# Kernel tuning notes

Hardware: AMD Instinct MI355X
Metric: run time of the kernel (lower is better)

## Reference

```python
import jax, jax.numpy as jnp
import numpy as np

N_SR = 50000; N_TG = 50000; DIM = 256; VAL_DIM = 300; ATT_NUM = 1001
N_VAL = 100000; E_ATTR = 200000; E_EDGE = 400000; N_SEED = 10000


def _build_adj(rng, n, e):
    # replicate preprocess_adj: symmetrize, add self-loops, coalesce + clamp(values,1)
    edges = rng.integers(0, n, size=(e, 2))
    und = np.concatenate([edges, edges[:, ::-1]], axis=0)
    loops = np.repeat(np.arange(n)[:, None], 2, axis=1)
    uniq = np.unique(np.concatenate([und, loops], axis=0), axis=0)  # coalesced binary adj
    return jnp.asarray(uniq[:, 0], jnp.int32), jnp.asarray(uniq[:, 1], jnp.int32)


def _xavier(k, shape):
    fan_in, fan_out = shape[0], shape[-1]
    s = jnp.sqrt(6.0 / (fan_in + fan_out)).astype(jnp.float32)
    return jax.random.uniform(k, shape, jnp.float32, -1.0, 1.0) * s


def setup_inputs():
    rng = np.random.default_rng(0)
    ks = jax.random.split(jax.random.key(0), 10)

    def triples(n_ent):
        return jnp.asarray(np.stack([rng.integers(0, n_ent, E_ATTR),
                                     rng.integers(0, N_VAL, E_ATTR),
                                     rng.integers(0, ATT_NUM, E_ATTR)], axis=1), jnp.int32)

    r_sr, c_sr = _build_adj(rng, N_SR, E_EDGE)
    r_tg, c_tg = _build_adj(rng, N_TG, E_EDGE)
    return {
        'ent_seed_sr': jnp.asarray(rng.integers(0, N_SR, N_SEED), jnp.int32),
        'ent_seed_tg': jnp.asarray(rng.integers(0, N_TG, N_SEED), jnp.int32),
        'attribute_triples_sr': triples(N_SR),
        'attribute_triples_tg': triples(N_TG),
        'adj_rows_sr': r_sr, 'adj_cols_sr': c_sr,
        'adj_rows_tg': r_tg, 'adj_cols_tg': c_tg,
        'att_feats': _xavier(ks[0], (ATT_NUM, DIM)),
        'val_feats': jax.random.normal(ks[1], (N_VAL, VAL_DIM), jnp.float32),
        'ent_feats_sr': _xavier(ks[2], (N_SR, DIM)),
        'ent_feats_tg': _xavier(ks[3], (N_TG, DIM)),
        'a_w': _xavier(ks[4], (2 * DIM, 1)).reshape(-1),
        'a_b': jnp.zeros((1,), jnp.float32),
        'W_enc': _xavier(ks[5], (DIM + VAL_DIM, DIM)),
        'gcn_w1': _xavier(ks[6], (DIM, DIM)),
        'gcn_b1': jnp.zeros((DIM,), jnp.float32),
        'gcn_w2': _xavier(ks[7], (DIM, DIM)),
        'gcn_b2': jnp.zeros((DIM,), jnp.float32),
    }


def attributed_encoder(triples, att_feats, val_feats, ent_feats, a_w, a_b, W_enc):
    h, val, att = triples[:, 0], triples[:, 1], triples[:, 2]
    n = ent_feats.shape[0]
    # edge attention score: Linear(cat(ent[h], att[att])) -> exp(leaky_relu(.))
    score = jnp.concatenate([ent_feats[h], att_feats[att]], axis=-1) @ a_w + a_b[0]  # [E]
    score = jnp.exp(jax.nn.leaky_relu(score, negative_slope=0.2))
    row_sum = jax.ops.segment_sum(score, h, num_segments=n)      # sparse softmax denom
    p = score / row_sum[h]                                       # [E]
    av = jnp.concatenate([att_feats[att], val_feats[val]], axis=-1) @ W_enc  # [E, DIM]
    agg = jax.ops.segment_sum(av * p[:, None], h, num_segments=n)
    return jax.nn.elu(agg + ent_feats)


def gcn_layer(rows, cols, feats, w, b, act):
    n = feats.shape[0]
    agg = jax.ops.segment_sum(feats[cols], rows, num_segments=n)           # A @ feats
    deg = jax.ops.segment_sum(jnp.ones(rows.shape, feats.dtype), rows, num_segments=n)
    h = act((agg / deg[:, None]) @ w + b)
    return feats + h  # residual, dims match


def _l2norm(x):
    return x / jnp.maximum(jnp.linalg.norm(x, axis=-1, keepdims=True), 1e-12)


def reference(ent_seed_sr, ent_seed_tg, attribute_triples_sr, attribute_triples_tg,
              adj_rows_sr, adj_cols_sr, adj_rows_tg, adj_cols_tg,
              att_feats, val_feats, ent_feats_sr, ent_feats_tg,
              a_w, a_b, W_enc, gcn_w1, gcn_b1, gcn_w2, gcn_b2):
    fs = attributed_encoder(attribute_triples_sr, att_feats, val_feats, ent_feats_sr, a_w, a_b, W_enc)
    ft = attributed_encoder(attribute_triples_tg, att_feats, val_feats, ent_feats_tg, a_w, a_b, W_enc)
    fs = gcn_layer(adj_rows_sr, adj_cols_sr, fs, gcn_w1, gcn_b1, jax.nn.relu)
    ft = gcn_layer(adj_rows_tg, adj_cols_tg, ft, gcn_w1, gcn_b1, jax.nn.relu)
    fs = gcn_layer(adj_rows_sr, adj_cols_sr, fs, gcn_w2, gcn_b2, lambda x: x)
    ft = gcn_layer(adj_rows_tg, adj_cols_tg, ft, gcn_w2, gcn_b2, lambda x: x)
    fs = _l2norm(fs)
    ft = _l2norm(ft)
    return fs[ent_seed_sr], ft[ent_seed_tg], fs, ft
```

## Files before the change

kernel.cpp:

```cpp
#include <hip/hip_runtime.h>
#include <math.h>

#define DIM 256
#define VAL_DIM 300

typedef __attribute__((ext_vector_type(8))) short short8;
typedef __attribute__((ext_vector_type(4))) float fx4;
typedef _Float16 f16;
typedef __attribute__((ext_vector_type(4))) _Float16 h4;

__device__ __forceinline__ short f2bf(float x) {
    unsigned u = __float_as_uint(x);
    unsigned r = (u + 0x7fff + ((u >> 16) & 1)) >> 16;
    return (short)r;
}
__device__ __forceinline__ float bf2f(short h) {
    return __uint_as_float(((unsigned)(unsigned short)h) << 16);
}

__global__ void k_split_b(const float* __restrict__ W, short* __restrict__ Bhi,
                          short* __restrict__ Blo, int Kreal, int Kp, int Ncols) {
    int idx = blockIdx.x * 256 + threadIdx.x;
    int total = (Ncols / 16) * (Kp / 32) * 64;
    if (idx >= total) return;
    int lane = idx & 63;
    int kt = (idx >> 6) % (Kp / 32);
    int nt = (idx >> 6) / (Kp / 32);
    int n = nt * 16 + (lane & 15);
    int kbase = kt * 32 + ((lane >> 4) & 3) * 8;
    short h[8], l[8];
#pragma unroll
    for (int j = 0; j < 8; ++j) {
        int k = kbase + j;
        float x = (k < Kreal) ? W[(size_t)k * Ncols + n] : 0.f;
        short hh = f2bf(x);
        float r = x - bf2f(hh);
        h[j] = hh;
        l[j] = f2bf(r);
    }
    size_t base = (size_t)idx * 8;
#pragma unroll
    for (int j = 0; j < 8; ++j) { Bhi[base + j] = h[j]; Blo[base + j] = l[j]; }
}

template <int MODE>
__global__ void k_gemm(const float* __restrict__ A, const short* __restrict__ Bhi,
                       const short* __restrict__ Blo, const float* __restrict__ bias,
                       float* __restrict__ Out, f16* __restrict__ Out16, int M, int K, int Kp) {
    __shared__ short Ah[8 * 512];
    __shared__ short Al[8 * 512];
    const int m0 = blockIdx.x * 64;
    const int tid = threadIdx.x;
    const int wave = tid >> 6;
    const int lane = tid & 63;
    const int wm = wave >> 2;
    const int wn = wave & 3;
    fx4 acc[2][4] = {};

    for (int pk = 0; pk < Kp; pk += 64) {
        {
            int ss = tid;
            int mt = ss >> 7;
            int ks = (ss >> 6) & 1;
            int ln = ss & 63;
            int row = m0 + mt * 16 + (ln & 15);
            int kk = pk + ks * 32 + ((ln >> 4) & 3) * 8;
            float v[8];
            if (row < M && kk + 8 <= K) {
                fx4 u0 = *(const fx4*)&A[(size_t)row * K + kk];
                fx4 u1 = *(const fx4*)&A[(size_t)row * K + kk + 4];
                v[0] = u0[0]; v[1] = u0[1]; v[2] = u0[2]; v[3] = u0[3];
                v[4] = u1[0]; v[5] = u1[1]; v[6] = u1[2]; v[7] = u1[3];
            } else {
#pragma unroll
                for (int j = 0; j < 8; ++j)
                    v[j] = (row < M && kk + j < K) ? A[(size_t)row * K + kk + j] : 0.f;
            }
            short8 h8, l8;
#pragma unroll
            for (int j = 0; j < 8; ++j) {
                short hh = f2bf(v[j]);
                h8[j] = hh;
                l8[j] = f2bf(v[j] - bf2f(hh));
            }
            *(short8*)&Ah[(mt * 2 + ks) * 512 + ln * 8] = h8;
            *(short8*)&Al[(mt * 2 + ks) * 512 + ln * 8] = l8;
        }
        __syncthreads();
#pragma unroll
        for (int ks = 0; ks < 2; ++ks) {
            int kglob = pk + ks * 32;
            short8 ah[2], al[2], bh[4], bl[4];
#pragma unroll
            for (int t = 0; t < 2; ++t) {
                ah[t] = *(short8*)&Ah[((wm * 2 + t) * 2 + ks) * 512 + lane * 8];
                al[t] = *(short8*)&Al[((wm * 2 + t) * 2 + ks) * 512 + lane * 8];
            }
#pragma unroll
            for (int t = 0; t < 4; ++t) {
                int ntg = wn * 4 + t;
                size_t fb = ((size_t)(ntg * (Kp >> 5) + (kglob >> 5))) * 512 + lane * 8;
                bh[t] = *(const short8*)&Bhi[fb];
                bl[t] = *(const short8*)&Blo[fb];
            }
#pragma unroll
            for (int i = 0; i < 2; ++i)
#pragma unroll
                for (int j = 0; j < 4; ++j) {
                    acc[i][j] = __builtin_amdgcn_mfma_f32_16x16x32_bf16(ah[i], bh[j], acc[i][j], 0, 0, 0);
                    acc[i][j] = __builtin_amdgcn_mfma_f32_16x16x32_bf16(ah[i], bl[j], acc[i][j], 0, 0, 0);
                    acc[i][j] = __builtin_amdgcn_mfma_f32_16x16x32_bf16(al[i], bh[j], acc[i][j], 0, 0, 0);
                }
        }
        __syncthreads();
    }
    const int quad = lane >> 4;
    const int cl = lane & 15;
#pragma unroll
    for (int i = 0; i < 2; ++i) {
        int rbase = m0 + (wm * 2 + i) * 16 + quad * 4;
#pragma unroll
        for (int j = 0; j < 4; ++j) {
            int col = (wn * 4 + j) * 16 + cl;
            float bb = (MODE == 0) ? 0.f : bias[col];
#pragma unroll
            for (int r = 0; r < 4; ++r) {
                int row = rbase + r;
                if (row >= M) continue;
                size_t idx = (size_t)row * DIM + col;
                if (MODE == 0) {
                    Out16[idx] = (f16)acc[i][j][r];
                } else if (MODE == 1) {
                    float h = fmaxf(acc[i][j][r] + bb, 0.f);
                    float v = Out[idx] + h;
                    Out[idx] = v;
                    Out16[idx] = (f16)v;
                } else {
                    Out[idx] += acc[i][j][r] + bb;
                }
            }
        }
    }
}

__global__ void k_att(const float* __restrict__ att_feats, const float* __restrict__ W_enc,
                      const float* __restrict__ a_w, float* __restrict__ att_proj,
                      float* __restrict__ att_score) {
    int a = blockIdx.x;
    int j = threadIdx.x;
    __shared__ float row[DIM];
    __shared__ float red[DIM];
    float v = att_feats[a * DIM + j];
    row[j] = v;
    red[j] = v * a_w[DIM + j];
    __syncthreads();
    for (int s = 128; s > 0; s >>= 1) {
        if (j < s) red[j] += red[j + s];
        __syncthreads();
    }
    if (j == 0) att_score[a] = red[0];
    float acc = 0.f;
    for (int d = 0; d < DIM; ++d)
        acc += row[d] * W_enc[d * DIM + j];
    att_proj[a * DIM + j] = acc;
}

__global__ void k_ent_score(const float* __restrict__ ent, const float* __restrict__ a_w,
                            float* __restrict__ score) {
    int i = blockIdx.x;
    int j = threadIdx.x;
    __shared__ float red[DIM];
    red[j] = ent[(size_t)i * DIM + j] * a_w[j];
    __syncthreads();
    for (int s = 128; s > 0; s >>= 1) {
        if (j < s) red[j] += red[j + s];
        __syncthreads();
    }
    if (j == 0) score[i] = red[0];
}

__global__ void k_edge_score(const int* __restrict__ triples, const float* __restrict__ ent_score,
                             const float* __restrict__ att_score, const float* __restrict__ a_b,
                             float* __restrict__ edge_w, float* __restrict__ row_sum,
                             int* __restrict__ cnt, int* __restrict__ rank, int e_attr) {
    int e = blockIdx.x * blockDim.x + threadIdx.x;
    if (e >= e_attr) return;
    int h = triples[e * 3 + 0];
    int att = triples[e * 3 + 2];
    float s = ent_score[h] + att_score[att] + a_b[0];
    s = (s >= 0.f) ? s : 0.2f * s;
    float w = expf(s);
    edge_w[e] = w;
    atomicAdd(&row_sum[h], w);
    rank[e] = atomicAdd(&cnt[h], 1);
}

__global__ void k_blocksum(const int* __restrict__ cnt, int* __restrict__ bsum, int n) {
    int i = blockIdx.x * 256 + threadIdx.x;
    int v = (i < n) ? cnt[i] : 0;
    __shared__ int red[256];
    red[threadIdx.x] = v;
    __syncthreads();
    for (int s = 128; s > 0; s >>= 1) {
        if (threadIdx.x < s) red[threadIdx.x] += red[threadIdx.x + s];
        __syncthreads();
    }
    if (threadIdx.x == 0) bsum[blockIdx.x] = red[0];
}

__global__ void k_scan_bsum(int* __restrict__ bsum, int nb) {
    int t = threadIdx.x;
    int v = (t < nb) ? bsum[t] : 0;
    __shared__ int buf[256];
    buf[t] = v;
    __syncthreads();
    for (int s = 1; s < 256; s <<= 1) {
        int tv = (t >= s) ? buf[t - s] : 0;
        __syncthreads();
        buf[t] += tv;
        __syncthreads();
    }
    if (t < nb) bsum[t] = buf[t] - v;
}

__global__ void k_scan_final(const int* __restrict__ cnt, const int* __restrict__ bsum,
                             int* __restrict__ off, int n) {
    int b = blockIdx.x;
    int t = threadIdx.x;
    int i = b * 256 + t;
    int v = (i < n) ? cnt[i] : 0;
    __shared__ int buf[256];
    buf[t] = v;
    __syncthreads();
    for (int s = 1; s < 256; s <<= 1) {
        int tv = (t >= s) ? buf[t - s] : 0;
        __syncthreads();
        buf[t] += tv;
        __syncthreads();
    }
    if (i < n) off[i] = bsum[b] + buf[t] - v;
    if (i == n - 1) off[n] = bsum[b] + buf[t];
}

__global__ void k_scatter(const int* __restrict__ triples, const int* __restrict__ rank,
                          const int* __restrict__ off, int* __restrict__ eidx, int e_attr) {
    int e = blockIdx.x * blockDim.x + threadIdx.x;
    if (e >= e_attr) return;
    int h = triples[e * 3 + 0];
    eidx[off[h] + rank[e]] = e;
}

__global__ void k_edge_agg_csr(const int* __restrict__ triples, const float* __restrict__ edge_w,
                               const float* __restrict__ row_sum, const int* __restrict__ off,
                               const int* __restrict__ eidx, const fx4* __restrict__ att_proj,
                               const h4* __restrict__ val_proj, const fx4* __restrict__ ent,
                               fx4* __restrict__ F, h4* __restrict__ F16, int n) {
    int wave = threadIdx.x >> 6;
    int lane = threadIdx.x & 63;
    int h = blockIdx.x * 4 + wave;
    if (h >= n) return;
    int s = off[h], e = off[h + 1];
    fx4 acc = {};
    float inv = (e > s) ? 1.0f / row_sum[h] : 0.f;
    for (int j = s; j < e; ++j) {
        int ed = eidx[j];
        int val = triples[ed * 3 + 1];
        int att = triples[ed * 3 + 2];
        float p = edge_w[ed] * inv;
        fx4 a = att_proj[(size_t)att * 64 + lane];
        h4 v = val_proj[(size_t)val * 64 + lane];
#pragma unroll
        for (int c = 0; c < 4; ++c) acc[c] += p * (a[c] + (float)v[c]);
    }
    fx4 x = acc + ent[(size_t)h * 64 + lane];
    fx4 r;
    h4 r16;
#pragma unroll
    for (int c = 0; c < 4; ++c) {
        r[c] = (x[c] > 0.f) ? x[c] : expm1f(x[c]);
        r16[c] = (f16)r[c];
    }
    F[(size_t)h * 64 + lane] = r;
    F16[(size_t)h * 64 + lane] = r16;
}

__global__ void k_deg(const int* __restrict__ rows, int n_edges, int n,
                      int* __restrict__ off, float* __restrict__ deg_inv) {
    int i = blockIdx.x * blockDim.x + threadIdx.x;
    if (i > n) return;
    int lo = 0, hi = n_edges;
    while (lo < hi) {
        int m = (lo + hi) >> 1;
        if (rows[m] < i) lo = m + 1; else hi = m;
    }
    off[i] = lo;
    if (i < n) {
        int lo2 = lo, hi2 = n_edges;
        while (lo2 < hi2) {
            int m = (lo2 + hi2) >> 1;
            if (rows[m] < i + 1) lo2 = m + 1; else hi2 = m;
        }
        int d = lo2 - lo;
        deg_inv[i] = 1.0f / (float)(d > 0 ? d : 1);
    }
}

__global__ void k_gcn_agg(const int* __restrict__ off, const int* __restrict__ cols,
                          const float* __restrict__ deg_inv, const h4* __restrict__ F16,
                          fx4* __restrict__ T, int n) {
    int wave = threadIdx.x >> 6;
    int lane = threadIdx.x & 63;
    int i = blockIdx.x * 4 + wave;
    if (i >= n) return;
    int s = off[i], e = off[i + 1];
    fx4 acc = {};
    int k = s;
    for (; k + 4 <= e; k += 4) {
        int c0 = cols[k], c1 = cols[k + 1], c2 = cols[k + 2], c3 = cols[k + 3];
        h4 r0 = F16[(size_t)c0 * 64 + lane];
        h4 r1 = F16[(size_t)c1 * 64 + lane];
        h4 r2 = F16[(size_t)c2 * 64 + lane];
        h4 r3 = F16[(size_t)c3 * 64 + lane];
#pragma unroll
        for (int c = 0; c < 4; ++c)
            acc[c] += ((float)r0[c] + (float)r1[c]) + ((float)r2[c] + (float)r3[c]);
    }
    for (; k < e; ++k) {
        h4 r = F16[(size_t)cols[k] * 64 + lane];
#pragma unroll
        for (int c = 0; c < 4; ++c) acc[c] += (float)r[c];
    }
    T[(size_t)i * 64 + lane] = acc * deg_inv[i];
}

__global__ void k_norm_out(const float* __restrict__ F, float* __restrict__ out) {
    int i = blockIdx.x;
    int j = threadIdx.x;
    __shared__ float red[DIM];
    float v = F[(size_t)i * DIM + j];
    red[j] = v * v;
    __syncthreads();
    for (int s = 128; s > 0; s >>= 1) {
        if (j < s) red[j] += red[j + s];
        __syncthreads();
    }
    float sc = 1.0f / fmaxf(sqrtf(red[0]), 1e-12f);
    out[(size_t)i * DIM + j] = v * sc;
}

__global__ void k_gather(const int* __restrict__ seed, const float* __restrict__ full,
                         float* __restrict__ out) {
    int i = blockIdx.x;
    int j = threadIdx.x;
    out[(size_t)i * DIM + j] = full[(size_t)seed[i] * DIM + j];
}

extern "C" void kernel_launch(void* const* d_in, const int* in_sizes, int n_in,
                              void* d_out, int out_size, void* d_ws, size_t ws_size,
                              hipStream_t stream) {
    const int* seed_sr = (const int*)d_in[0];
    const int* seed_tg = (const int*)d_in[1];
    const int* tri_sr = (const int*)d_in[2];
    const int* tri_tg = (const int*)d_in[3];
    const int* rows_sr = (const int*)d_in[4];
    const int* cols_sr = (const int*)d_in[5];
    const int* rows_tg = (const int*)d_in[6];
    const int* cols_tg = (const int*)d_in[7];
    const float* att_feats = (const float*)d_in[8];
    const float* val_feats = (const float*)d_in[9];
    const float* ent_sr = (const float*)d_in[10];
    const float* ent_tg = (const float*)d_in[11];
    const float* a_w = (const float*)d_in[12];
    const float* a_b = (const float*)d_in[13];
    const float* W_enc = (const float*)d_in[14];
    const float* w1 = (const float*)d_in[15];
    const float* b1 = (const float*)d_in[16];
    const float* w2 = (const float*)d_in[17];
    const float* b2 = (const float*)d_in[18];

    const int N = in_sizes[10] / DIM;
    const int n_att = in_sizes[8] / DIM;
    const int n_val = in_sizes[9] / VAL_DIM;
    const int e_attr = in_sizes[2] / 3;
    const int n_seed = in_sizes[0];
    const int KpV = 320;
    const int nb = (N + 255) / 256;

    char* p = (char*)d_ws;
    auto alloc = [&](size_t nbytes) -> void* {
        void* r = (void*)p;
        p += (nbytes + 255) & ~(size_t)255;
        return r;
    };
    f16* val16 = (f16*)alloc(sizeof(f16) * (size_t)n_val * DIM);
    float* att_proj = (float*)alloc(sizeof(float) * (size_t)n_att * DIM);
    float* att_score = (float*)alloc(sizeof(float) * (size_t)n_att);
    float* ent_score = (float*)alloc(sizeof(float) * (size_t)N);
    float* row_sum = (float*)alloc(sizeof(float) * (size_t)N);
    float* edge_w = (float*)alloc(sizeof(float) * (size_t)e_attr);
    float* deg_inv = (float*)alloc(sizeof(float) * (size_t)N);
    int* off = (int*)alloc(sizeof(int) * (size_t)(N + 1));
    int* off_csr = (int*)alloc(sizeof(int) * (size_t)(N + 1));
    int* cnt = (int*)alloc(sizeof(int) * (size_t)N);
    int* rank = (int*)alloc(sizeof(int) * (size_t)e_attr);
    int* bsum = (int*)alloc(sizeof(int) * (size_t)nb);
    int* eidx = (int*)alloc(sizeof(int) * (size_t)e_attr);
    float* F = (float*)alloc(sizeof(float) * (size_t)N * DIM);
    f16* F16 = (f16*)alloc(sizeof(f16) * (size_t)N * DIM);
    float* T = (float*)alloc(sizeof(float) * (size_t)N * DIM);
    short* wencv_hi = (short*)alloc(sizeof(short) * (DIM / 16) * (KpV / 32) * 512);
    short* wencv_lo = (short*)alloc(sizeof(short) * (DIM / 16) * (KpV / 32) * 512);
    short* w1_hi = (short*)alloc(sizeof(short) * (DIM / 16) * (DIM / 32) * 512);
    short* w1_lo = (short*)alloc(sizeof(short) * (DIM / 16) * (DIM / 32) * 512);
    short* w2_hi = (short*)alloc(sizeof(short) * (DIM / 16) * (DIM / 32) * 512);
    short* w2_lo = (short*)alloc(sizeof(short) * (DIM / 16) * (DIM / 32) * 512);

    float* out = (float*)d_out;
    float* out_seed_arr[2] = { out, out + (size_t)n_seed * DIM };
    float* out_full_arr[2] = { out + (size_t)2 * n_seed * DIM,
                               out + (size_t)2 * n_seed * DIM + (size_t)N * DIM };

    {
        int tot_v = (DIM / 16) * (KpV / 32) * 64;
        k_split_b<<<(tot_v + 255) / 256, 256, 0, stream>>>(W_enc + (size_t)DIM * DIM, wencv_hi,
                                                           wencv_lo, VAL_DIM, KpV, DIM);
        int tot_w = (DIM / 16) * (DIM / 32) * 64;
        k_split_b<<<(tot_w + 255) / 256, 256, 0, stream>>>(w1, w1_hi, w1_lo, DIM, DIM, DIM);
        k_split_b<<<(tot_w + 255) / 256, 256, 0, stream>>>(w2, w2_hi, w2_lo, DIM, DIM, DIM);
    }

    k_att<<<n_att, DIM, 0, stream>>>(att_feats, W_enc, a_w, att_proj, att_score);
    k_gemm<0><<<(n_val + 63) / 64, 512, 0, stream>>>(val_feats, wencv_hi, wencv_lo, nullptr,
                                                     nullptr, val16, n_val, VAL_DIM, KpV);

    const int* tris[2] = { tri_sr, tri_tg };
    const float* ents[2] = { ent_sr, ent_tg };
    const int* rws[2] = { rows_sr, rows_tg };
    const int* cls[2] = { cols_sr, cols_tg };
    const int eadj[2] = { in_sizes[4], in_sizes[6] };
    const int* seeds[2] = { seed_sr, seed_tg };

    for (int s = 0; s < 2; ++s) {
        k_ent_score<<<N, DIM, 0, stream>>>(ents[s], a_w, ent_score);
        hipMemsetAsync(row_sum, 0, sizeof(float) * (size_t)N, stream);
        hipMemsetAsync(cnt, 0, sizeof(int) * (size_t)N, stream);
        k_edge_score<<<(e_attr + 255) / 256, 256, 0, stream>>>(tris[s], ent_score, att_score,
                                                               a_b, edge_w, row_sum, cnt, rank,
                                                               e_attr);
        k_blocksum<<<nb, 256, 0, stream>>>(cnt, bsum, N);
        k_scan_bsum<<<1, 256, 0, stream>>>(bsum, nb);
        k_scan_final<<<nb, 256, 0, stream>>>(cnt, bsum, off_csr, N);
        k_scatter<<<(e_attr + 255) / 256, 256, 0, stream>>>(tris[s], rank, off_csr, eidx, e_attr);
        k_edge_agg_csr<<<(N + 3) / 4, 256, 0, stream>>>(tris[s], edge_w, row_sum, off_csr, eidx,
                                                        (const fx4*)att_proj, (const h4*)val16,
                                                        (const fx4*)ents[s], (fx4*)F, (h4*)F16, N);
        k_deg<<<(N + 1 + 255) / 256, 256, 0, stream>>>(rws[s], eadj[s], N, off, deg_inv);
        k_gcn_agg<<<(N + 3) / 4, 256, 0, stream>>>(off, cls[s], deg_inv, (const h4*)F16, (fx4*)T, N);
        k_gemm<1><<<(N + 63) / 64, 512, 0, stream>>>(T, w1_hi, w1_lo, b1, F, F16, N, DIM, DIM);
        k_gcn_agg<<<(N + 3) / 4, 256, 0, stream>>>(off, cls[s], deg_inv, (const h4*)F16, (fx4*)T, N);
        k_gemm<2><<<(N + 63) / 64, 512, 0, stream>>>(T, w2_hi, w2_lo, b2, F, nullptr, N, DIM, DIM);
        k_norm_out<<<N, DIM, 0, stream>>>(F, out_full_arr[s]);
        k_gather<<<n_seed, DIM, 0, stream>>>(seeds[s], out_full_arr[s], out_seed_arr[s]);
    }
}
```

Measured before the change: 1.174 ms.

## Double-buffer A panels in GEMM to overlap global loads with MFMA

The GEMM kernel now keeps two LDS buffers for the split bf16 A panel. It prefetches the next K-panel from global memory into registers before the MFMA loop over the current buffer, then writes it to the other buffer, which drops one barrier per iteration. The B-fragment loads are also moved inside the MFMA loop, so fewer B registers are live at once. The cost is twice the LDS footprint and extra registers for the prefetched values, which may lower occupancy.

```diff
diff --git a/kernel.cpp b/kernel.cpp
--- a/kernel.cpp
+++ b/kernel.cpp
@@ -47,72 +47,83 @@
 __global__ void k_gemm(const float* __restrict__ A, const short* __restrict__ Bhi,
                        const short* __restrict__ Blo, const float* __restrict__ bias,
                        float* __restrict__ Out, f16* __restrict__ Out16, int M, int K, int Kp) {
-    __shared__ short Ah[8 * 512];
-    __shared__ short Al[8 * 512];
+    __shared__ short Ah[2][8 * 512];
+    __shared__ short Al[2][8 * 512];
     const int m0 = blockIdx.x * 64;
     const int tid = threadIdx.x;
     const int wave = tid >> 6;
     const int lane = tid & 63;
     const int wm = wave >> 2;
     const int wn = wave & 3;
+    const int smt = tid >> 7;
+    const int sks = (tid >> 6) & 1;
+    const int sln = tid & 63;
+    const int srow = m0 + smt * 16 + (sln & 15);
+    const int skoff = sks * 32 + ((sln >> 4) & 3) * 8;
+    const int sdst = (smt * 2 + sks) * 512 + sln * 8;
     fx4 acc[2][4] = {};
 
+    float v[8];
+    auto load_panel = [&](int pk, float* dst) {
+        int kk = pk + skoff;
+        if (srow < M && kk + 8 <= K) {
+            fx4 u0 = *(const fx4*)&A[(size_t)srow * K + kk];
+            fx4 u1 = *(const fx4*)&A[(size_t)srow * K + kk + 4];
+            dst[0] = u0[0]; dst[1] = u0[1]; dst[2] = u0[2]; dst[3] = u0[3];
+            dst[4] = u1[0]; dst[5] = u1[1]; dst[6] = u1[2]; dst[7] = u1[3];
+        } else {
+#pragma unroll
+            for (int j = 0; j < 8; ++j)
+                dst[j] = (srow < M && kk + j < K) ? A[(size_t)srow * K + kk + j] : 0.f;
+        }
+    };
+    auto store_panel = [&](int buf, const float* src) {
+        short8 h8, l8;
+#pragma unroll
+        for (int j = 0; j < 8; ++j) {
+            short hh = f2bf(src[j]);
+            h8[j] = hh;
+            l8[j] = f2bf(src[j] - bf2f(hh));
+        }
+        *(short8*)&Ah[buf][sdst] = h8;
+        *(short8*)&Al[buf][sdst] = l8;
+    };
+
+    load_panel(0, v);
+    store_panel(0, v);
+    __syncthreads();
+
+    int cur = 0;
     for (int pk = 0; pk < Kp; pk += 64) {
-        {
-            int ss = tid;
-            int mt = ss >> 7;
-            int ks = (ss >> 6) & 1;
-            int ln = ss & 63;
-            int row = m0 + mt * 16 + (ln & 15);
-            int kk = pk + ks * 32 + ((ln >> 4) & 3) * 8;
-            float v[8];
-            if (row < M && kk + 8 <= K) {
-                fx4 u0 = *(const fx4*)&A[(size_t)row * K + kk];
-                fx4 u1 = *(const fx4*)&A[(size_t)row * K + kk + 4];
-                v[0] = u0[0]; v[1] = u0[1]; v[2] = u0[2]; v[3] = u0[3];
-                v[4] = u1[0]; v[5] = u1[1]; v[6] = u1[2]; v[7] = u1[3];
-            } else {
-#pragma unroll
-                for (int j = 0; j < 8; ++j)
-                    v[j] = (row < M && kk + j < K) ? A[(size_t)row * K + kk + j] : 0.f;
-            }
-            short8 h8, l8;
-#pragma unroll
-            for (int j = 0; j < 8; ++j) {
-                short hh = f2bf(v[j]);
-                h8[j] = hh;
-                l8[j] = f2bf(v[j] - bf2f(hh));
-            }
-            *(short8*)&Ah[(mt * 2 + ks) * 512 + ln * 8] = h8;
-            *(short8*)&Al[(mt * 2 + ks) * 512 + ln * 8] = l8;
-        }
-        __syncthreads();
+        const bool more = (pk + 64) < Kp;
+        float nv[8];
+        if (more) load_panel(pk + 64, nv);
 #pragma unroll
         for (int ks = 0; ks < 2; ++ks) {
             int kglob = pk + ks * 32;
-            short8 ah[2], al[2], bh[4], bl[4];
+            short8 ah[2], al[2];
 #pragma unroll
             for (int t = 0; t < 2; ++t) {
-                ah[t] = *(short8*)&Ah[((wm * 2 + t) * 2 + ks) * 512 + lane * 8];
-                al[t] = *(short8*)&Al[((wm * 2 + t) * 2 + ks) * 512 + lane * 8];
+                ah[t] = *(short8*)&Ah[cur][((wm * 2 + t) * 2 + ks) * 512 + lane * 8];
+                al[t] = *(short8*)&Al[cur][((wm * 2 + t) * 2 + ks) * 512 + lane * 8];
             }
 #pragma unroll
-            for (int t = 0; t < 4; ++t) {
-                int ntg = wn * 4 + t;
+            for (int j = 0; j < 4; ++j) {
+                int ntg = wn * 4 + j;
                 size_t fb = ((size_t)(ntg * (Kp >> 5) + (kglob >> 5))) * 512 + lane * 8;
-                bh[t] = *(const short8*)&Bhi[fb];
-                bl[t] = *(const short8*)&Blo[fb];
+                short8 bh = *(const short8*)&Bhi[fb];
+                short8 bl = *(const short8*)&Blo[fb];
+#pragma unroll
+                for (int i = 0; i < 2; ++i) {
+                    acc[i][j] = __builtin_amdgcn_mfma_f32_16x16x32_bf16(ah[i], bh, acc[i][j], 0, 0, 0);
+                    acc[i][j] = __builtin_amdgcn_mfma_f32_16x16x32_bf16(ah[i], bl, acc[i][j], 0, 0, 0);
+                    acc[i][j] = __builtin_amdgcn_mfma_f32_16x16x32_bf16(al[i], bh, acc[i][j], 0, 0, 0);
+                }
             }
-#pragma unroll
-            for (int i = 0; i < 2; ++i)
-#pragma unroll
-                for (int j = 0; j < 4; ++j) {
-                    acc[i][j] = __builtin_amdgcn_mfma_f32_16x16x32_bf16(ah[i], bh[j], acc[i][j], 0, 0, 0);
-                    acc[i][j] = __builtin_amdgcn_mfma_f32_16x16x32_bf16(ah[i], bl[j], acc[i][j], 0, 0, 0);
-                    acc[i][j] = __builtin_amdgcn_mfma_f32_16x16x32_bf16(al[i], bh[j], acc[i][j], 0, 0, 0);
-                }
         }
-        __syncthreads();
+        if (more) store_panel(cur ^ 1, nv);
+        __syncthreads();
+        cur ^= 1;
     }
     const int quad = lane >> 4;
     const int cl = lane & 15;
@@ -132,9 +143,9 @@
                     Out16[idx] = (f16)acc[i][j][r];
                 } else if (MODE == 1) {
                     float h = fmaxf(acc[i][j][r] + bb, 0.f);
-                    float v = Out[idx] + h;
-                    Out[idx] = v;
-                    Out16[idx] = (f16)v;
+                    float vv = Out[idx] + h;
+                    Out[idx] = vv;
+                    Out16[idx] = (f16)vv;
                 } else {
                     Out[idx] += acc[i][j][r] + bb;
                 }
```

New measurement: 1.211 ms. 1.03x slower.

## Slice GCN aggregation by feature columns to improve cache locality of gathers

Applied to the files above, without the earlier changes.

Replaces the one-wave-per-row GCN aggregation with a kernel where each block handles 64 rows and one of eight 32-column feature slices. Within a wave, eight lane groups each take a different neighbor edge and reduce via cross-lane shuffles. Each pass touches only a 64-byte slice of every F16 row, so the gathered working set is smaller and should stay in cache across blocks working on the same slice. The cost is that edge indices are read eight times, rows with few neighbors leave lanes idle, and each block processes its rows serially.

```diff
diff --git a/kernel.cpp b/kernel.cpp
--- a/kernel.cpp
+++ b/kernel.cpp
@@ -3,6 +3,7 @@
 
 #define DIM 256
 #define VAL_DIM 300
+#define RPB 64
 
 typedef __attribute__((ext_vector_type(8))) short short8;
 typedef __attribute__((ext_vector_type(4))) float fx4;
@@ -132,9 +133,9 @@
                     Out16[idx] = (f16)acc[i][j][r];
                 } else if (MODE == 1) {
                     float h = fmaxf(acc[i][j][r] + bb, 0.f);
-                    float v = Out[idx] + h;
-                    Out[idx] = v;
-                    Out16[idx] = (f16)v;
+                    float vv = Out[idx] + h;
+                    Out[idx] = vv;
+                    Out16[idx] = (f16)vv;
                 } else {
                     Out[idx] += acc[i][j][r] + bb;
                 }
@@ -305,32 +306,41 @@
     }
 }
 
-__global__ void k_gcn_agg(const int* __restrict__ off, const int* __restrict__ cols,
-                          const float* __restrict__ deg_inv, const h4* __restrict__ F16,
-                          fx4* __restrict__ T, int n) {
+__global__ void k_gcn_agg_sliced(const int* __restrict__ off, const int* __restrict__ cols,
+                                 const float* __restrict__ deg_inv, const h4* __restrict__ F16,
+                                 fx4* __restrict__ T, int n) {
+    int b = blockIdx.x;
+    int sl = b & 7;
+    int rb = b >> 3;
     int wave = threadIdx.x >> 6;
-    int lane = threadIdx.x & 63;
-    int i = blockIdx.x * 4 + wave;
-    if (i >= n) return;
-    int s = off[i], e = off[i + 1];
-    fx4 acc = {};
-    int k = s;
-    for (; k + 4 <= e; k += 4) {
-        int c0 = cols[k], c1 = cols[k + 1], c2 = cols[k + 2], c3 = cols[k + 3];
-        h4 r0 = F16[(size_t)c0 * 64 + lane];
-        h4 r1 = F16[(size_t)c1 * 64 + lane];
-        h4 r2 = F16[(size_t)c2 * 64 + lane];
-        h4 r3 = F16[(size_t)c3 * 64 + lane];
-#pragma unroll
-        for (int c = 0; c < 4; ++c)
-            acc[c] += ((float)r0[c] + (float)r1[c]) + ((float)r2[c] + (float)r3[c]);
-    }
-    for (; k < e; ++k) {
-        h4 r = F16[(size_t)cols[k] * 64 + lane];
-#pragma unroll
-        for (int c = 0; c < 4; ++c) acc[c] += (float)r[c];
-    }
-    T[(size_t)i * 64 + lane] = acc * deg_inv[i];
+    int l = threadIdx.x & 63;
+    int g = l >> 3;
+    int sub = l & 7;
+    int row_end = rb * RPB + RPB;
+    if (row_end > n) row_end = n;
+    for (int i = rb * RPB + wave; i < row_end; i += 4) {
+        int s = off[i], e = off[i + 1];
+        fx4 acc = {};
+        for (int e0 = s; e0 < e; e0 += 8) {
+            int ee = e0 + g;
+            if (ee < e) {
+                int c = cols[ee];
+                h4 r = F16[(size_t)c * 64 + sl * 8 + sub];
+                acc[0] += (float)r[0];
+                acc[1] += (float)r[1];
+                acc[2] += (float)r[2];
+                acc[3] += (float)r[3];
+            }
+        }
+#pragma unroll
+        for (int m = 8; m <= 32; m <<= 1) {
+            acc[0] += __shfl_xor(acc[0], m, 64);
+            acc[1] += __shfl_xor(acc[1], m, 64);
+            acc[2] += __shfl_xor(acc[2], m, 64);
+            acc[3] += __shfl_xor(acc[3], m, 64);
+        }
+        if (g == 0) T[(size_t)i * 64 + sl * 8 + sub] = acc * deg_inv[i];
+    }
 }
 
 __global__ void k_norm_out(const float* __restrict__ F, float* __restrict__ out) {
@@ -440,6 +450,8 @@
     const int eadj[2] = { in_sizes[4], in_sizes[6] };
     const int* seeds[2] = { seed_sr, seed_tg };
 
+    const int g_sliced = 8 * ((N + RPB - 1) / RPB);
+
     for (int s = 0; s < 2; ++s) {
         k_ent_score<<<N, DIM, 0, stream>>>(ents[s], a_w, ent_score);
         hipMemsetAsync(row_sum, 0, sizeof(float) * (size_t)N, stream);
@@ -455,9 +467,11 @@
                                                         (const fx4*)att_proj, (const h4*)val16,
                                                         (const fx4*)ents[s], (fx4*)F, (h4*)F16, N);
         k_deg<<<(N + 1 + 255) / 256, 256, 0, stream>>>(rws[s], eadj[s], N, off, deg_inv);
-        k_gcn_agg<<<(N + 3) / 4, 256, 0, stream>>>(off, cls[s], deg_inv, (const h4*)F16, (fx4*)T, N);
+        k_gcn_agg_sliced<<<g_sliced, 256, 0, stream>>>(off, cls[s], deg_inv, (const h4*)F16,
+                                                       (fx4*)T, N);
         k_gemm<1><<<(N + 63) / 64, 512, 0, stream>>>(T, w1_hi, w1_lo, b1, F, F16, N, DIM, DIM);
-        k_gcn_agg<<<(N + 3) / 4, 256, 0, stream>>>(off, cls[s], deg_inv, (const h4*)F16, (fx4*)T, N);
+        k_gcn_agg_sliced<<<g_sliced, 256, 0, stream>>>(off, cls[s], deg_inv, (const h4*)F16,
+                                                       (fx4*)T, N);
         k_gemm<2><<<(N + 63) / 64, 512, 0, stream>>>(T, w2_hi, w2_lo, b2, F, nullptr, N, DIM, DIM);
         k_norm_out<<<N, DIM, 0, stream>>>(F, out_full_arr[s]);
         k_gather<<<n_seed, DIM, 0, stream>>>(seeds[s], out_full_arr[s], out_seed_arr[s]);
```

Result: slower. 1.572 ms (+33.8%).

## Fuse GCN neighbor aggregation into the GEMM via shared-memory bf16 split tiles

Applied to the files above, without the earlier changes.

Replaces the separate gather-aggregate kernel, which wrote an fp32 intermediate T, with a fused kernel. Each block aggregates 64 rows' neighbor features directly into shared memory as hi/lo bf16 splits, then runs the MFMA GEMM with bias/residual epilogue. This removes the write and read of the N×256 fp32 intermediate and two launches per graph. The layer-1 fp16 output goes to a separate buffer so layer 2 can read it without a race. The fused kernel uses about 64 KB of LDS per block, which limits occupancy, and the gather phase is latency bound with only 8 waves per block.

```diff
diff --git a/kernel.cpp b/kernel.cpp
--- a/kernel.cpp
+++ b/kernel.cpp
@@ -5,6 +5,7 @@
 #define VAL_DIM 300
 
 typedef __attribute__((ext_vector_type(8))) short short8;
+typedef __attribute__((ext_vector_type(4))) short short4v;
 typedef __attribute__((ext_vector_type(4))) float fx4;
 typedef _Float16 f16;
 typedef __attribute__((ext_vector_type(4))) _Float16 h4;
@@ -122,19 +123,119 @@
 #pragma unroll
         for (int j = 0; j < 4; ++j) {
             int col = (wn * 4 + j) * 16 + cl;
-            float bb = (MODE == 0) ? 0.f : bias[col];
+#pragma unroll
+            for (int r = 0; r < 4; ++r) {
+                int row = rbase + r;
+                if (row >= M) continue;
+                Out16[(size_t)row * DIM + col] = (f16)acc[i][j][r];
+            }
+        }
+    }
+}
+
+template <int MODE>
+__global__ void k_gcn_gemm(const int* __restrict__ off, const int* __restrict__ cols,
+                           const float* __restrict__ deg_inv, const h4* __restrict__ Fin16,
+                           const short* __restrict__ Bhi, const short* __restrict__ Blo,
+                           const float* __restrict__ bias, float* __restrict__ Out,
+                           f16* __restrict__ Out16, int M) {
+    __shared__ short Ah[32 * 512];
+    __shared__ short Al[32 * 512];
+    const int m0 = blockIdx.x * 64;
+    const int tid = threadIdx.x;
+    const int wave = tid >> 6;
+    const int lane = tid & 63;
+
+    for (int rr = wave * 8; rr < wave * 8 + 8; ++rr) {
+        int row = m0 + rr;
+        if (row >= M) break;
+        int s = off[row], e = off[row + 1];
+        fx4 acc = {};
+        int k = s;
+        for (; k + 4 <= e; k += 4) {
+            int c0 = cols[k], c1 = cols[k + 1], c2 = cols[k + 2], c3 = cols[k + 3];
+            h4 r0 = Fin16[(size_t)c0 * 64 + lane];
+            h4 r1 = Fin16[(size_t)c1 * 64 + lane];
+            h4 r2 = Fin16[(size_t)c2 * 64 + lane];
+            h4 r3 = Fin16[(size_t)c3 * 64 + lane];
+#pragma unroll
+            for (int c = 0; c < 4; ++c)
+                acc[c] += ((float)r0[c] + (float)r1[c]) + ((float)r2[c] + (float)r3[c]);
+        }
+        for (; k < e; ++k) {
+            h4 r = Fin16[(size_t)cols[k] * 64 + lane];
+#pragma unroll
+            for (int c = 0; c < 4; ++c) acc[c] += (float)r[c];
+        }
+        float di = deg_inv[row];
+        int k0 = lane * 4;
+        int sub = (rr >> 4) * 8 + (k0 >> 6) * 2 + ((k0 >> 5) & 1);
+        int ln = ((k0 >> 3) & 3) * 16 + (rr & 15);
+        int j = k0 & 7;
+        short4v hv, lv;
+#pragma unroll
+        for (int c = 0; c < 4; ++c) {
+            float x = acc[c] * di;
+            short hh = f2bf(x);
+            hv[c] = hh;
+            lv[c] = f2bf(x - bf2f(hh));
+        }
+        *(short4v*)&Ah[sub * 512 + ln * 8 + j] = hv;
+        *(short4v*)&Al[sub * 512 + ln * 8 + j] = lv;
+    }
+    __syncthreads();
+
+    const int wm = wave >> 2;
+    const int wn = wave & 3;
+    fx4 acc[2][4] = {};
+#pragma unroll
+    for (int p = 0; p < 4; ++p) {
+#pragma unroll
+        for (int ks = 0; ks < 2; ++ks) {
+            int ktile = p * 2 + ks;
+            short8 ah[2], al[2], bh[4], bl[4];
+#pragma unroll
+            for (int t = 0; t < 2; ++t) {
+                int sub = (wm * 2 + t) * 8 + ktile;
+                ah[t] = *(short8*)&Ah[sub * 512 + lane * 8];
+                al[t] = *(short8*)&Al[sub * 512 + lane * 8];
+            }
+#pragma unroll
+            for (int t = 0; t < 4; ++t) {
+                int ntg = wn * 4 + t;
+                size_t fb = ((size_t)(ntg * 8 + ktile)) * 512 + lane * 8;
+                bh[t] = *(const short8*)&Bhi[fb];
+                bl[t] = *(const short8*)&Blo[fb];
+            }
+#pragma unroll
+            for (int i = 0; i < 2; ++i)
+#pragma unroll
+                for (int j = 0; j < 4; ++j) {
+                    acc[i][j] = __builtin_amdgcn_mfma_f32_16x16x32_bf16(ah[i], bh[j], acc[i][j], 0, 0, 0);
+                    acc[i][j] = __builtin_amdgcn_mfma_f32_16x16x32_bf16(ah[i], bl[j], acc[i][j], 0, 0, 0);
+                    acc[i][j] = __builtin_amdgcn_mfma_f32_16x16x32_bf16(al[i], bh[j], acc[i][j], 0, 0, 0);
+                }
+        }
+    }
+    const int quad = lane >> 4;
+    const int cl = lane & 15;
+#pragma unroll
+    for (int i = 0; i < 2; ++i) {
+        int rbase = m0 + (wm * 2 + i) * 16 + quad * 4;
+#pragma unroll
+        for (int j = 0; j < 4; ++j) {
+            int col = (wn * 4 + j) * 16 + cl;
+            float bb = bias[col];
 #pragma unroll
             for (int r = 0; r < 4; ++r) {
                 int row = rbase + r;
                 if (row >= M) continue;
                 size_t idx = (size_t)row * DIM + col;
-                if (MODE == 0) {
-                    Out16[idx] = (f16)acc[i][j][r];
-                } else if (MODE == 1) {
+                if (MODE == 1) {
                     float h = fmaxf(acc[i][j][r] + bb, 0.f);
-                    float v = Out[idx] + h;
-                    Out[idx] = v;
-                    Out16[idx] = (f16)v;
+                    float vv = Out[idx] + h;
+                    Out[idx] = vv;
+                    Out16[idx] = (f16)vv;
                 } else {
                     Out[idx] += acc[i][j][r] + bb;
                 }
@@ -303,34 +404,6 @@
         int d = lo2 - lo;
         deg_inv[i] = 1.0f / (float)(d > 0 ? d : 1);
     }
-}
-
-__global__ void k_gcn_agg(const int* __restrict__ off, const int* __restrict__ cols,
-                          const float* __restrict__ deg_inv, const h4* __restrict__ F16,
-                          fx4* __restrict__ T, int n) {
-    int wave = threadIdx.x >> 6;
-    int lane = threadIdx.x & 63;
-    int i = blockIdx.x * 4 + wave;
-    if (i >= n) return;
-    int s = off[i], e = off[i + 1];
-    fx4 acc = {};
-    int k = s;
-    for (; k + 4 <= e; k += 4) {
-        int c0 = cols[k], c1 = cols[k + 1], c2 = cols[k + 2], c3 = cols[k + 3];
-        h4 r0 = F16[(size_t)c0 * 64 + lane];
-        h4 r1 = F16[(size_t)c1 * 64 + lane];
-        h4 r2 = F16[(size_t)c2 * 64 + lane];
-        h4 r3 = F16[(size_t)c3 * 64 + lane];
-#pragma unroll
-        for (int c = 0; c < 4; ++c)
-            acc[c] += ((float)r0[c] + (float)r1[c]) + ((float)r2[c] + (float)r3[c]);
-    }
-    for (; k < e; ++k) {
-        h4 r = F16[(size_t)cols[k] * 64 + lane];
-#pragma unroll
-        for (int c = 0; c < 4; ++c) acc[c] += (float)r[c];
-    }
-    T[(size_t)i * 64 + lane] = acc * deg_inv[i];
 }
 
 __global__ void k_norm_out(const float* __restrict__ F, float* __restrict__ out) {
@@ -407,7 +480,7 @@
     int* eidx = (int*)alloc(sizeof(int) * (size_t)e_attr);
     float* F = (float*)alloc(sizeof(float) * (size_t)N * DIM);
     f16* F16 = (f16*)alloc(sizeof(f16) * (size_t)N * DIM);
-    float* T = (float*)alloc(sizeof(float) * (size_t)N * DIM);
+    f16* F16b = (f16*)alloc(sizeof(f16) * (size_t)N * DIM);
     short* wencv_hi = (short*)alloc(sizeof(short) * (DIM / 16) * (KpV / 32) * 512);
     short* wencv_lo = (short*)alloc(sizeof(short) * (DIM / 16) * (KpV / 32) * 512);
     short* w1_hi = (short*)alloc(sizeof(short) * (DIM / 16) * (DIM / 32) * 512);
@@ -455,10 +528,10 @@
                                                         (const fx4*)att_proj, (const h4*)val16,
                                                         (const fx4*)ents[s], (fx4*)F, (h4*)F16, N);
         k_deg<<<(N + 1 + 255) / 256, 256, 0, stream>>>(rws[s], eadj[s], N, off, deg_inv);
-        k_gcn_agg<<<(N + 3) / 4, 256, 0, stream>>>(off, cls[s], deg_inv, (const h4*)F16, (fx4*)T, N);
-        k_gemm<1><<<(N + 63) / 64, 512, 0, stream>>>(T, w1_hi, w1_lo, b1, F, F16, N, DIM, DIM);
-        k_gcn_agg<<<(N + 3) / 4, 256, 0, stream>>>(off, cls[s], deg_inv, (const h4*)F16, (fx4*)T, N);
-        k_gemm<2><<<(N + 63) / 64, 512, 0, stream>>>(T, w2_hi, w2_lo, b2, F, nullptr, N, DIM, DIM);
+        k_gcn_gemm<1><<<(N + 63) / 64, 512, 0, stream>>>(off, cls[s], deg_inv, (const h4*)F16,
+                                                         w1_hi, w1_lo, b1, F, F16b, N);
+        k_gcn_gemm<2><<<(N + 63) / 64, 512, 0, stream>>>(off, cls[s], deg_inv, (const h4*)F16b,
+                                                         w2_hi, w2_lo, b2, F, nullptr, N);
         k_norm_out<<<N, DIM, 0, stream>>>(F, out_full_arr[s]);
         k_gather<<<n_seed, DIM, 0, stream>>>(seeds[s], out_full_arr[s], out_seed_arr[s]);
     }
```

Result: slower. 1.215 ms (+3.4%).
